# Kernel tuning notes

Measured on AMD Instinct MI355X. Metric: run time of the kernel, lower is better.

The kernel has to match this reference:

```python
import jax, jax.numpy as jnp
import numpy as np

B, S, C = 2, 2048, 512
L, H, CH = 4, 8, 64  # layers, heads, per-head channel (H*CH == C)
OD = 4 * CH          # GEGLU output_dim = channel*4 = 256
EPS = 1e-5


def layer_norm(x, g, b):
    mu = jnp.mean(x, axis=-1, keepdims=True)
    var = jnp.mean(jnp.square(x - mu), axis=-1, keepdims=True)
    return (x - mu) * jax.lax.rsqrt(var + EPS) * g + b


def gelu_tanh(g):
    # matches: 0.5 * g * (1 + tanh(g * 0.7978845608 * (1 + 0.044715 * g**2)))
    t = jnp.tanh(g * 0.7978845608 * (1.0 + 0.044715 * jnp.square(g)))
    return 0.5 * g * (1.0 + t)


def setup_inputs() -> dict:
    key = jax.random.key(0)
    ks = jax.random.split(key, 8)
    s = 0.02
    return {
        "x": jax.random.normal(ks[0], (B, S, C), jnp.float32),
        "ln_gamma": jnp.ones((L + 1, C), jnp.float32),
        "ln_beta": jnp.zeros((L + 1, C), jnp.float32),
        "Wq": jax.random.normal(ks[1], (L, C, H * CH), jnp.float32) * s,
        "Wk": jax.random.normal(ks[2], (L, C, H * CH), jnp.float32) * s,
        "Wv": jax.random.normal(ks[3], (L, C, H * CH), jnp.float32) * s,
        "Wo": jax.random.normal(ks[4], (L, H * CH, C), jnp.float32) * s,
        "bo": jnp.zeros((L, C), jnp.float32),
        "Wg": jax.random.normal(ks[5], (C, 2 * OD), jnp.float32) * s,
        "bg": jnp.zeros((2 * OD,), jnp.float32),
        "Wf": jax.random.normal(ks[6], (OD, C), jnp.float32) * s,
        "bf": jnp.zeros((C,), jnp.float32),
    }


def reference(x, ln_gamma, ln_beta, Wq, Wk, Wv, Wo, bo, Wg, bg, Wf, bf):
    scale = 1.0 / jnp.sqrt(jnp.asarray(CH, x.dtype))
    for i in range(L):
        h = layer_norm(x, ln_gamma[i], ln_beta[i])
        q = (h @ Wq[i]).reshape(B, S, H, CH)
        k = (h @ Wk[i]).reshape(B, S, H, CH)
        v = (h @ Wv[i]).reshape(B, S, H, CH)
        scores = jnp.einsum("bqhc,bkhc->bhqk", q, k) * scale
        w = jax.nn.softmax(scores, axis=-1)
        o = jnp.einsum("bhqk,bkhc->bqhc", w, v).reshape(B, S, H * CH)
        x = o @ Wo[i] + bo[i] + x
    h = layer_norm(x, ln_gamma[L], ln_beta[L])
    g = h @ Wg + bg
    a, gate = g[..., :OD], g[..., OD:]
    ff = a * gelu_tanh(gate)
    return ff @ Wf + bf + x
```

## Files before the change

### kernel.cpp

```cpp
#include <hip/hip_runtime.h>
#include <hip/hip_bf16.h>


typedef __bf16 bf16_t;
typedef __attribute__((ext_vector_type(8))) __bf16 bf16x8;
typedef __attribute__((ext_vector_type(4))) __bf16 bf16x4;
typedef __attribute__((ext_vector_type(4))) float f32x4;

#define MROWS 4096
#define KVSPLIT 2
#define NT 16

static __device__ __forceinline__ void gload_lds16(const void* g, void* l) {
  __builtin_amdgcn_global_load_lds((const __attribute__((address_space(1))) void*)g,
                                   (__attribute__((address_space(3))) void*)l, 16, 0, 0);
}
static __device__ __forceinline__ float fexp2(float x) {
  float r;
  asm("v_exp_f32 %0, %1" : "=v"(r) : "v"(x));
  return r;
}

__global__ __launch_bounds__(256) void ln_kernel(const float* __restrict__ xin,
    const float* __restrict__ gamma, const float* __restrict__ beta,
    bf16_t* __restrict__ hout)
{
  int w = threadIdx.x >> 6, l = threadIdx.x & 63;
  int row = blockIdx.x * 4 + w;
  const float* xr = xin + (size_t)row * 512 + l * 8;
  f32x4 a = *(const f32x4*)xr;
  f32x4 b2 = *(const f32x4*)(xr + 4);
  float s = a[0]+a[1]+a[2]+a[3]+b2[0]+b2[1]+b2[2]+b2[3];
  #pragma unroll
  for (int m = 1; m < 64; m <<= 1) s += __shfl_xor(s, m, 64);
  float mu = s * (1.0f/512.0f);
  float vs = 0.f;
  #pragma unroll
  for (int i = 0; i < 4; i++) { float d = a[i]-mu; vs += d*d; d = b2[i]-mu; vs += d*d; }
  #pragma unroll
  for (int m = 1; m < 64; m <<= 1) vs += __shfl_xor(vs, m, 64);
  float rstd = rsqrtf(vs * (1.0f/512.0f) + 1e-5f);
  const float* gp = gamma + l*8;
  const float* bp = beta + l*8;
  f32x4 g0 = *(const f32x4*)gp, g1 = *(const f32x4*)(gp+4);
  f32x4 p0 = *(const f32x4*)bp, p1 = *(const f32x4*)(bp+4);
  bf16x8 h;
  #pragma unroll
  for (int i = 0; i < 4; i++) {
    h[i]   = (bf16_t)((a[i]-mu)*rstd*g0[i] + p0[i]);
    h[4+i] = (bf16_t)((b2[i]-mu)*rstd*g1[i] + p1[i]);
  }
  *(bf16x8*)(hout + (size_t)row*512 + l*8) = h;
}

__global__ __launch_bounds__(256) void prep_kernel(
    const float* __restrict__ Wq, const float* __restrict__ Wk, const float* __restrict__ Wv,
    const float* __restrict__ Wo, const float* __restrict__ Wg, const float* __restrict__ Wf,
    bf16_t* __restrict__ WqkvT, bf16_t* __restrict__ WoT,
    bf16_t* __restrict__ WgT, bf16_t* __restrict__ WfT)
{
  __shared__ float tile[32][33];
  int z = blockIdx.z;
  const float* src; bf16_t* dst; int K = 512, N = 512;
  if (z < 12) {
    int lay = z & 3, which = z >> 2;
    src = (which == 0 ? Wq : which == 1 ? Wk : Wv) + (size_t)lay*512*512;
    dst = WqkvT + (size_t)lay*1536*512 + (size_t)which*512*512;
  } else if (z < 16) {
    src = Wo + (size_t)(z-12)*512*512;
    dst = WoT + (size_t)(z-12)*512*512;
  } else if (z == 16) { src = Wg; dst = WgT; }
  else { src = Wf; dst = WfT; K = 256; }
  int k0 = blockIdx.y*32, n0 = blockIdx.x*32;
  if (k0 >= K) return;
  int tx = threadIdx.x & 31, ty = threadIdx.x >> 5;
  #pragma unroll
  for (int j = 0; j < 4; j++)
    tile[ty + j*8][tx] = src[(size_t)(k0 + ty + j*8)*N + n0 + tx];
  __syncthreads();
  #pragma unroll
  for (int j = 0; j < 4; j++)
    dst[(size_t)(n0 + ty + j*8)*K + k0 + tx] = (bf16_t)tile[tx][ty + j*8];
}

template<int EPI, int BM, int NX>
__global__ __launch_bounds__(256) void gemm_bt(
    const bf16_t* __restrict__ A, const bf16_t* __restrict__ Bt,
    int N, int K,
    void* __restrict__ Cout, bf16_t* __restrict__ vTout,
    const float* __restrict__ bias, const float* __restrict__ resid, float qscale)
{
  __shared__ bf16_t As[BM*64];
  __shared__ bf16_t Bs[128*64];
  constexpr int MF = BM/32;
  int cpx = gridDim.x >> 3;
  int logical = (blockIdx.x & 7) * cpx + (blockIdx.x >> 3);
  int bx = logical % NX, by = logical / NX;
  int t = threadIdx.x, w = t >> 6, l = t & 63;
  int tm = by * BM, tn = bx * 128;
  int wm = (w >> 1) * (BM/2), wn = (w & 1) * 64;
  f32x4 acc[MF][4] = {};
  int srow = l >> 3;
  int schunk = ((l & 7) ^ srow) * 8;
  for (int k0 = 0; k0 < K; k0 += 64) {
    __syncthreads();
    #pragma unroll
    for (int i = 0; i < BM/32; i++) {
      int rb = i*32 + w*8;
      gload_lds16(A + (size_t)(tm + rb + srow)*K + k0 + schunk, &As[rb*64]);
    }
    #pragma unroll
    for (int i = 0; i < 4; i++) {
      int rb = i*32 + w*8;
      gload_lds16(Bt + (size_t)(tn + rb + srow)*K + k0 + schunk, &Bs[rb*64]);
    }
    __syncthreads();
    #pragma unroll
    for (int kk = 0; kk < 2; kk++) {
      bf16x8 af[MF], bfr[4];
      #pragma unroll
      for (int mf = 0; mf < MF; mf++) {
        int row = wm + mf*16 + (l & 15);
        int off = (kk*32 + (l >> 4)*8) ^ ((row & 7) << 3);
        af[mf] = *(const bf16x8*)&As[row*64 + off];
      }
      #pragma unroll
      for (int nf = 0; nf < 4; nf++) {
        int row = wn + nf*16 + (l & 15);
        int off = (kk*32 + (l >> 4)*8) ^ ((row & 7) << 3);
        bfr[nf] = *(const bf16x8*)&Bs[row*64 + off];
      }
      #pragma unroll
      for (int mf = 0; mf < MF; mf++)
        #pragma unroll
        for (int nf = 0; nf < 4; nf++)
          acc[mf][nf] = __builtin_amdgcn_mfma_f32_16x16x32_bf16(af[mf], bfr[nf], acc[mf][nf], 0, 0, 0);
    }
  }
  int colb = tn + wn + (l & 15);
  int rowb = tm + wm + ((l >> 4) << 2);
  if (EPI == 0 && tn >= 1024) {
    #pragma unroll
    for (int mf = 0; mf < MF; mf++)
      #pragma unroll
      for (int nf = 0; nf < 4; nf++) {
        int col = colb + nf*16;
        int hh = (col - 1024) >> 6, ch = (col - 1024) & 63;
        int row = rowb + mf*16;
        int bb = row >> 11, sdx = row & 2047;
        bf16x4 pk;
        #pragma unroll
        for (int r = 0; r < 4; r++) pk[r] = (bf16_t)acc[mf][nf][r];
        *(bf16x4*)&vTout[(((size_t)bb*8 + hh)*64 + ch)*2048 + sdx] = pk;
      }
    return;
  }
  #pragma unroll
  for (int mf = 0; mf < MF; mf++)
    #pragma unroll
    for (int nf = 0; nf < 4; nf++)
      #pragma unroll
      for (int r = 0; r < 4; r++) {
        int row = rowb + mf*16 + r;
        int col = colb + nf*16;
        float v = acc[mf][nf][r];
        if (EPI == 0) {
          if (col < 512) v *= qscale;
          ((bf16_t*)Cout)[(size_t)row*1024 + col] = (bf16_t)v;
        } else if (EPI == 1) {
          ((float*)Cout)[(size_t)row*N + col] = v + bias[col] + resid[(size_t)row*N + col];
        } else {
          ((float*)Cout)[(size_t)row*N + col] = v + bias[col];
        }
      }
}

__global__ __launch_bounds__(256) void attn_kernel(const bf16_t* __restrict__ qkv,
                                                   const bf16_t* __restrict__ vT,
                                                   bf16_t* __restrict__ Ows,
                                                   float* __restrict__ lws)
{
  __shared__ bf16_t Ks[64*64];
  __shared__ bf16_t Vs[64*64];
  __shared__ bf16_t Ps[4*16*72];
  int t = threadIdx.x, w = t >> 6, l = t & 63;
  int logical = (blockIdx.x & 7) * 128 + (blockIdx.x >> 3);
  int q0 = (logical & 31) * 64;
  int group = logical >> 5;
  int h = group & 7;
  int bz = group >> 3;
  int b = bz >> 1, sp = bz & 1;
  size_t rbase = (size_t)b * 2048;
  int kvb = sp * (2048/KVSPLIT);
  int lq = l & 15, hi = l >> 4;
  int srow = l >> 3;
  int schunk = ((l & 7) ^ srow) * 8;
  int rb0 = w*16, rb1 = w*16 + 8;
  const bf16_t* kb  = qkv + rbase*1024 + 512 + h*64;
  const bf16_t* vtb = vT + ((size_t)(b*8 + h)*64)*2048 + kvb;
  const bf16_t* qp = qkv + (rbase + q0 + w*16 + lq)*1024 + h*64 + hi*8;
  bf16x8 aq0 = *(const bf16x8*)qp;
  bf16x8 aq1 = *(const bf16x8*)(qp + 32);
  gload_lds16(kb + (size_t)(kvb + rb0 + srow)*1024 + schunk, &Ks[rb0*64]);
  gload_lds16(kb + (size_t)(kvb + rb1 + srow)*1024 + schunk, &Ks[rb1*64]);
  gload_lds16(vtb + (size_t)(rb0 + srow)*2048 + schunk, &Vs[rb0*64]);
  gload_lds16(vtb + (size_t)(rb1 + srow)*2048 + schunk, &Vs[rb1*64]);
  asm volatile("s_waitcnt vmcnt(0)" ::: "memory");
  __builtin_amdgcn_s_barrier();

  int pw = w * 16 * 72;
  f32x4 accO[4] = {};
  f32x4 lacc = {};
  bf16x8 ones;
  #pragma unroll
  for (int e = 0; e < 8; e++) ones[e] = (bf16_t)1.0f;
  int swz = (lq & 7) << 3;

  for (int tt = 0; tt < NT; ++tt) {
    f32x4 s4[4] = {};
    bf16x8 vv[8];
    #pragma unroll
    for (int kk = 0; kk < 2; kk++) {
      int off = (kk*32 + hi*8) ^ swz;
      bf16x8 aq = kk ? aq1 : aq0;
      #pragma unroll
      for (int nf = 0; nf < 4; nf++) {
        bf16x8 bk = *(const bf16x8*)&Ks[(nf*16 + lq)*64 + off];
        s4[nf] = __builtin_amdgcn_mfma_f32_16x16x32_bf16(aq, bk, s4[nf], 0, 0, 0);
        vv[kk*4+nf] = *(const bf16x8*)&Vs[(nf*16 + lq)*64 + off];
      }
    }
    asm volatile("s_waitcnt lgkmcnt(0)" ::: "memory");
    __builtin_amdgcn_s_barrier();
    __builtin_amdgcn_sched_barrier(0);
    if (tt < NT-1) {
      int kv1 = kvb + (tt + 1) * 64;
      gload_lds16(kb + (size_t)(kv1 + rb0 + srow)*1024 + schunk, &Ks[rb0*64]);
      gload_lds16(kb + (size_t)(kv1 + rb1 + srow)*1024 + schunk, &Ks[rb1*64]);
      gload_lds16(vtb + (size_t)(rb0 + srow)*2048 + (tt+1)*64 + schunk, &Vs[rb0*64]);
      gload_lds16(vtb + (size_t)(rb1 + srow)*2048 + (tt+1)*64 + schunk, &Vs[rb1*64]);
    }
    #pragma unroll
    for (int nf = 0; nf < 4; nf++)
      #pragma unroll
      for (int r = 0; r < 4; r++)
        Ps[pw + (hi*4 + r)*72 + nf*16 + lq] = (bf16_t)fexp2(s4[nf][r]);
    #pragma unroll
    for (int kk = 0; kk < 2; kk++) {
      bf16x8 pa = *(const bf16x8*)&Ps[pw + lq*72 + kk*32 + hi*8];
      lacc = __builtin_amdgcn_mfma_f32_16x16x32_bf16(pa, ones, lacc, 0, 0, 0);
      #pragma unroll
      for (int nf = 0; nf < 4; nf++)
        accO[nf] = __builtin_amdgcn_mfma_f32_16x16x32_bf16(pa, vv[kk*4+nf], accO[nf], 0, 0, 0);
    }
    if (tt < NT-1) {
      asm volatile("s_waitcnt vmcnt(0)" ::: "memory");
      __builtin_amdgcn_s_barrier();
    }
  }
  bf16_t* op = Ows + (size_t)sp*MROWS*512 + (rbase + q0 + w*16 + hi*4)*512 + h*64 + lq;
  #pragma unroll
  for (int nf = 0; nf < 4; nf++)
    #pragma unroll
    for (int r = 0; r < 4; r++)
      op[(size_t)r*512 + nf*16] = (bf16_t)accO[nf][r];
  if (lq == 0) {
    size_t rowb = rbase + q0 + w*16 + hi*4;
    #pragma unroll
    for (int r = 0; r < 4; r++)
      lws[(size_t)sp*MROWS*8 + (rowb + r)*8 + h] = lacc[r];
  }
}

__global__ __launch_bounds__(256) void combine_kernel(const bf16_t* __restrict__ Ows,
                                                      const float* __restrict__ lws,
                                                      bf16_t* __restrict__ obuf)
{
  int idx = blockIdx.x * 256 + threadIdx.x;
  int row = idx >> 7, c4 = (idx & 127) * 4;
  bf16x4 o0 = *(const bf16x4*)&Ows[(size_t)row*512 + c4];
  bf16x4 o1 = *(const bf16x4*)&Ows[(size_t)(MROWS + row)*512 + c4];
  int h = c4 >> 6;
  float li = 1.0f / (lws[row*8 + h] + lws[MROWS*8 + row*8 + h]);
  bf16x4 o;
  #pragma unroll
  for (int i = 0; i < 4; i++) o[i] = (bf16_t)(((float)o0[i] + (float)o1[i]) * li);
  *(bf16x4*)&obuf[(size_t)row*512 + c4] = o;
}

__global__ __launch_bounds__(256) void gelu_kernel(const float* __restrict__ g,
                                                   bf16_t* __restrict__ ff)
{
  int idx = blockIdx.x * 256 + threadIdx.x;
  int row = idx >> 6;
  int c = (idx & 63) * 4;
  const float* gr = g + (size_t)row*512;
  f32x4 a = *(const f32x4*)(gr + c);
  f32x4 u = *(const f32x4*)(gr + 256 + c);
  bf16x4 o4;
  #pragma unroll
  for (int i = 0; i < 4; i++) {
    float x = u[i];
    float tt = tanhf(0.7978845608f * x * (1.0f + 0.044715f * x * x));
    o4[i] = (bf16_t)(a[i] * 0.5f * x * (1.0f + tt));
  }
  *(bf16x4*)(ff + (size_t)row*256 + c) = o4;
}

extern "C" void kernel_launch(void* const* d_in, const int* in_sizes, int n_in,
                              void* d_out, int out_size, void* d_ws, size_t ws_size,
                              hipStream_t stream)
{
  const float* x     = (const float*)d_in[0];
  const float* gamma = (const float*)d_in[1];
  const float* beta  = (const float*)d_in[2];
  const float* Wq    = (const float*)d_in[3];
  const float* Wk    = (const float*)d_in[4];
  const float* Wv    = (const float*)d_in[5];
  const float* Wo    = (const float*)d_in[6];
  const float* bo    = (const float*)d_in[7];
  const float* Wg    = (const float*)d_in[8];
  const float* bg    = (const float*)d_in[9];
  const float* Wf    = (const float*)d_in[10];
  const float* bf    = (const float*)d_in[11];

  char* ws = (char*)d_ws;
  float*  xcur  = (float*)ws;
  bf16_t* hbuf  = (bf16_t*)(ws + (8u<<20));
  bf16_t* qkv   = (bf16_t*)(ws + (12u<<20));
  bf16_t* vT    = (bf16_t*)(ws + (20u<<20));
  bf16_t* obuf  = (bf16_t*)(ws + (24u<<20));
  bf16_t* WqkvT = (bf16_t*)(ws + (28u<<20));
  bf16_t* WoT   = (bf16_t*)(ws + (34u<<20));
  bf16_t* WgT   = (bf16_t*)(ws + (36u<<20));
  bf16_t* WfT   = (bf16_t*)(ws + (36u<<20) + (512u<<10));
  float*  lws   = (float*)(ws + (37u<<20));
  bf16_t* Ows   = (bf16_t*)(ws + (40u<<20));
  float*  gbuf  = (float*)qkv;
  bf16_t* ffb   = obuf;

  const float QSCALE = 0.125f * 1.44269504f;

  prep_kernel<<<dim3(16,16,18), 256, 0, stream>>>(Wq,Wk,Wv,Wo,Wg,Wf,WqkvT,WoT,WgT,WfT);
  hipMemcpyAsync(xcur, x, (size_t)MROWS*512*4, hipMemcpyDeviceToDevice, stream);

  for (int lay = 0; lay < 4; lay++) {
    ln_kernel<<<1024, 256, 0, stream>>>(xcur, gamma + lay*512, beta + lay*512, hbuf);
    gemm_bt<0,64,12><<<768, 256, 0, stream>>>(hbuf, WqkvT + (size_t)lay*1536*512,
                                              1536, 512, qkv, vT, nullptr, nullptr, QSCALE);
    attn_kernel<<<1024, 256, 0, stream>>>(qkv, vT, Ows, lws);
    combine_kernel<<<2048, 256, 0, stream>>>(Ows, lws, obuf);
    gemm_bt<1,64,4><<<256, 256, 0, stream>>>(obuf, WoT + (size_t)lay*512*512,
                                             512, 512, xcur, nullptr, bo + lay*512, xcur, 1.0f);
  }
  ln_kernel<<<1024, 256, 0, stream>>>(xcur, gamma + 4*512, beta + 4*512, hbuf);
  gemm_bt<2,64,4><<<256, 256, 0, stream>>>(hbuf, WgT, 512, 512, gbuf, nullptr, bg, nullptr, 1.0f);
  gelu_kernel<<<1024, 256, 0, stream>>>(gbuf, ffb);
  gemm_bt<1,64,4><<<256, 256, 0, stream>>>(ffb, WfT, 512, 256, d_out, nullptr, bf, xcur, 1.0f);
}
```

Baseline: 389.4 us.

## Store K and V in pre-tiled per-head blocks; double-buffer K, read V directly

The QKV GEMM epilogue now writes Q to its own buffer and writes K and V into contiguous per-(batch, head, 64-row tile) blocks. Attention can then stream K into a double-buffered LDS tile and load V fragments straight from global memory into registers, with no V staging in LDS. The change removes the mid-iteration barrier and the strided global loads, and it raises wave priority around the MFMA sections. The trade-offs are scattered 2-byte stores for K in the GEMM epilogue and V reads that come from global or cache on every iteration.

```diff
diff --git a/kernel.cpp b/kernel.cpp
--- a/kernel.cpp
+++ b/kernel.cpp
@@ -87,7 +87,7 @@
 __global__ __launch_bounds__(256) void gemm_bt(
     const bf16_t* __restrict__ A, const bf16_t* __restrict__ Bt,
     int N, int K,
-    void* __restrict__ Cout, bf16_t* __restrict__ vTout,
+    void* __restrict__ Cout, bf16_t* __restrict__ kTout, bf16_t* __restrict__ vTout,
     const float* __restrict__ bias, const float* __restrict__ resid, float qscale)
 {
   __shared__ bf16_t As[BM*64];
@@ -147,11 +147,27 @@
         int col = colb + nf*16;
         int hh = (col - 1024) >> 6, ch = (col - 1024) & 63;
         int row = rowb + mf*16;
-        int bb = row >> 11, sdx = row & 2047;
+        int bb = row >> 11, sin = row & 2047;
         bf16x4 pk;
         #pragma unroll
         for (int r = 0; r < 4; r++) pk[r] = (bf16_t)acc[mf][nf][r];
-        *(bf16x4*)&vTout[(((size_t)bb*8 + hh)*64 + ch)*2048 + sdx] = pk;
+        *(bf16x4*)&vTout[(((size_t)(bb*8 + hh)*32 + (sin >> 6))*64 + ch)*64 + (sin & 63)] = pk;
+      }
+    return;
+  }
+  if (EPI == 0 && tn >= 512) {
+    #pragma unroll
+    for (int mf = 0; mf < MF; mf++)
+      #pragma unroll
+      for (int nf = 0; nf < 4; nf++) {
+        int col = colb + nf*16;
+        int hh = (col - 512) >> 6, ch = (col - 512) & 63;
+        int row = rowb + mf*16;
+        int bb = row >> 11, sin = row & 2047;
+        size_t base = (((size_t)(bb*8 + hh)*32 + (sin >> 6))*64 + (sin & 63))*64 + ch;
+        #pragma unroll
+        for (int r = 0; r < 4; r++)
+          kTout[base + (size_t)r*64] = (bf16_t)acc[mf][nf][r];
       }
     return;
   }
@@ -165,8 +181,7 @@
         int col = colb + nf*16;
         float v = acc[mf][nf][r];
         if (EPI == 0) {
-          if (col < 512) v *= qscale;
-          ((bf16_t*)Cout)[(size_t)row*1024 + col] = (bf16_t)v;
+          ((bf16_t*)Cout)[(size_t)row*512 + col] = (bf16_t)(v * qscale);
         } else if (EPI == 1) {
           ((float*)Cout)[(size_t)row*N + col] = v + bias[col] + resid[(size_t)row*N + col];
         } else {
@@ -175,13 +190,13 @@
       }
 }
 
-__global__ __launch_bounds__(256) void attn_kernel(const bf16_t* __restrict__ qkv,
+__global__ __launch_bounds__(256) void attn_kernel(const bf16_t* __restrict__ qbuf,
+                                                   const bf16_t* __restrict__ kT,
                                                    const bf16_t* __restrict__ vT,
                                                    bf16_t* __restrict__ Ows,
                                                    float* __restrict__ lws)
 {
-  __shared__ bf16_t Ks[64*64];
-  __shared__ bf16_t Vs[64*64];
+  __shared__ bf16_t Ks[2][64*64];
   __shared__ bf16_t Ps[4*16*72];
   int t = threadIdx.x, w = t >> 6, l = t & 63;
   int logical = (blockIdx.x & 7) * 128 + (blockIdx.x >> 3);
@@ -191,20 +206,18 @@
   int bz = group >> 3;
   int b = bz >> 1, sp = bz & 1;
   size_t rbase = (size_t)b * 2048;
-  int kvb = sp * (2048/KVSPLIT);
   int lq = l & 15, hi = l >> 4;
   int srow = l >> 3;
   int schunk = ((l & 7) ^ srow) * 8;
   int rb0 = w*16, rb1 = w*16 + 8;
-  const bf16_t* kb  = qkv + rbase*1024 + 512 + h*64;
-  const bf16_t* vtb = vT + ((size_t)(b*8 + h)*64)*2048 + kvb;
-  const bf16_t* qp = qkv + (rbase + q0 + w*16 + lq)*1024 + h*64 + hi*8;
+  size_t tbase = ((size_t)(b*8 + h)*32 + sp*16) * 4096;
+  const bf16_t* kb = kT + tbase;
+  const bf16_t* vb = vT + tbase + (size_t)lq*64 + hi*8;
+  const bf16_t* qp = qbuf + (rbase + q0 + w*16 + lq)*512 + h*64 + hi*8;
   bf16x8 aq0 = *(const bf16x8*)qp;
   bf16x8 aq1 = *(const bf16x8*)(qp + 32);
-  gload_lds16(kb + (size_t)(kvb + rb0 + srow)*1024 + schunk, &Ks[rb0*64]);
-  gload_lds16(kb + (size_t)(kvb + rb1 + srow)*1024 + schunk, &Ks[rb1*64]);
-  gload_lds16(vtb + (size_t)(rb0 + srow)*2048 + schunk, &Vs[rb0*64]);
-  gload_lds16(vtb + (size_t)(rb1 + srow)*2048 + schunk, &Vs[rb1*64]);
+  gload_lds16(kb + (size_t)(rb0 + srow)*64 + schunk, &Ks[0][rb0*64]);
+  gload_lds16(kb + (size_t)(rb1 + srow)*64 + schunk, &Ks[0][rb1*64]);
   asm volatile("s_waitcnt vmcnt(0)" ::: "memory");
   __builtin_amdgcn_s_barrier();
 
@@ -217,34 +230,39 @@
   int swz = (lq & 7) << 3;
 
   for (int tt = 0; tt < NT; ++tt) {
+    int cur = tt & 1;
+    bf16x8 vv[8];
+    const bf16_t* vt0 = vb + (size_t)tt*4096;
+    #pragma unroll
+    for (int nf = 0; nf < 4; nf++) {
+      vv[nf]   = *(const bf16x8*)(vt0 + nf*1024);
+      vv[4+nf] = *(const bf16x8*)(vt0 + nf*1024 + 32);
+    }
+    if (tt < NT-1) {
+      const bf16_t* kn = kb + (size_t)(tt+1)*4096;
+      gload_lds16(kn + (size_t)(rb0 + srow)*64 + schunk, &Ks[cur^1][rb0*64]);
+      gload_lds16(kn + (size_t)(rb1 + srow)*64 + schunk, &Ks[cur^1][rb1*64]);
+    }
+    __builtin_amdgcn_sched_barrier(0);
     f32x4 s4[4] = {};
-    bf16x8 vv[8];
+    __builtin_amdgcn_s_setprio(1);
     #pragma unroll
     for (int kk = 0; kk < 2; kk++) {
       int off = (kk*32 + hi*8) ^ swz;
       bf16x8 aq = kk ? aq1 : aq0;
       #pragma unroll
       for (int nf = 0; nf < 4; nf++) {
-        bf16x8 bk = *(const bf16x8*)&Ks[(nf*16 + lq)*64 + off];
+        bf16x8 bk = *(const bf16x8*)&Ks[cur][(nf*16 + lq)*64 + off];
         s4[nf] = __builtin_amdgcn_mfma_f32_16x16x32_bf16(aq, bk, s4[nf], 0, 0, 0);
-        vv[kk*4+nf] = *(const bf16x8*)&Vs[(nf*16 + lq)*64 + off];
-      }
-    }
-    asm volatile("s_waitcnt lgkmcnt(0)" ::: "memory");
-    __builtin_amdgcn_s_barrier();
-    __builtin_amdgcn_sched_barrier(0);
-    if (tt < NT-1) {
-      int kv1 = kvb + (tt + 1) * 64;
-      gload_lds16(kb + (size_t)(kv1 + rb0 + srow)*1024 + schunk, &Ks[rb0*64]);
-      gload_lds16(kb + (size_t)(kv1 + rb1 + srow)*1024 + schunk, &Ks[rb1*64]);
-      gload_lds16(vtb + (size_t)(rb0 + srow)*2048 + (tt+1)*64 + schunk, &Vs[rb0*64]);
-      gload_lds16(vtb + (size_t)(rb1 + srow)*2048 + (tt+1)*64 + schunk, &Vs[rb1*64]);
-    }
+      }
+    }
+    __builtin_amdgcn_s_setprio(0);
     #pragma unroll
     for (int nf = 0; nf < 4; nf++)
       #pragma unroll
       for (int r = 0; r < 4; r++)
         Ps[pw + (hi*4 + r)*72 + nf*16 + lq] = (bf16_t)fexp2(s4[nf][r]);
+    __builtin_amdgcn_s_setprio(1);
     #pragma unroll
     for (int kk = 0; kk < 2; kk++) {
       bf16x8 pa = *(const bf16x8*)&Ps[pw + lq*72 + kk*32 + hi*8];
@@ -253,8 +271,9 @@
       for (int nf = 0; nf < 4; nf++)
         accO[nf] = __builtin_amdgcn_mfma_f32_16x16x32_bf16(pa, vv[kk*4+nf], accO[nf], 0, 0, 0);
     }
+    __builtin_amdgcn_s_setprio(0);
     if (tt < NT-1) {
-      asm volatile("s_waitcnt vmcnt(0)" ::: "memory");
+      asm volatile("s_waitcnt vmcnt(0) lgkmcnt(0)" ::: "memory");
       __builtin_amdgcn_s_barrier();
     }
   }
@@ -327,8 +346,9 @@
   char* ws = (char*)d_ws;
   float*  xcur  = (float*)ws;
   bf16_t* hbuf  = (bf16_t*)(ws + (8u<<20));
-  bf16_t* qkv   = (bf16_t*)(ws + (12u<<20));
-  bf16_t* vT    = (bf16_t*)(ws + (20u<<20));
+  bf16_t* qbuf  = (bf16_t*)(ws + (12u<<20));
+  bf16_t* kTb   = (bf16_t*)(ws + (16u<<20));
+  bf16_t* vTb   = (bf16_t*)(ws + (20u<<20));
   bf16_t* obuf  = (bf16_t*)(ws + (24u<<20));
   bf16_t* WqkvT = (bf16_t*)(ws + (28u<<20));
   bf16_t* WoT   = (bf16_t*)(ws + (34u<<20));
@@ -336,7 +356,7 @@
   bf16_t* WfT   = (bf16_t*)(ws + (36u<<20) + (512u<<10));
   float*  lws   = (float*)(ws + (37u<<20));
   bf16_t* Ows   = (bf16_t*)(ws + (40u<<20));
-  float*  gbuf  = (float*)qkv;
+  float*  gbuf  = (float*)(ws + (40u<<20));
   bf16_t* ffb   = obuf;
 
   const float QSCALE = 0.125f * 1.44269504f;
@@ -347,14 +367,14 @@
   for (int lay = 0; lay < 4; lay++) {
     ln_kernel<<<1024, 256, 0, stream>>>(xcur, gamma + lay*512, beta + lay*512, hbuf);
     gemm_bt<0,64,12><<<768, 256, 0, stream>>>(hbuf, WqkvT + (size_t)lay*1536*512,
-                                              1536, 512, qkv, vT, nullptr, nullptr, QSCALE);
-    attn_kernel<<<1024, 256, 0, stream>>>(qkv, vT, Ows, lws);
+                                              1536, 512, qbuf, kTb, vTb, nullptr, nullptr, QSCALE);
+    attn_kernel<<<1024, 256, 0, stream>>>(qbuf, kTb, vTb, Ows, lws);
     combine_kernel<<<2048, 256, 0, stream>>>(Ows, lws, obuf);
     gemm_bt<1,64,4><<<256, 256, 0, stream>>>(obuf, WoT + (size_t)lay*512*512,
-                                             512, 512, xcur, nullptr, bo + lay*512, xcur, 1.0f);
+                                             512, 512, xcur, nullptr, nullptr, bo + lay*512, xcur, 1.0f);
   }
   ln_kernel<<<1024, 256, 0, stream>>>(xcur, gamma + 4*512, beta + 4*512, hbuf);
-  gemm_bt<2,64,4><<<256, 256, 0, stream>>>(hbuf, WgT, 512, 512, gbuf, nullptr, bg, nullptr, 1.0f);
+  gemm_bt<2,64,4><<<256, 256, 0, stream>>>(hbuf, WgT, 512, 512, gbuf, nullptr, nullptr, bg, nullptr, 1.0f);
   gelu_kernel<<<1024, 256, 0, stream>>>(gbuf, ffb);
-  gemm_bt<1,64,4><<<256, 256, 0, stream>>>(ffb, WfT, 512, 256, d_out, nullptr, bf, xcur, 1.0f);
-}
+  gemm_bt<1,64,4><<<256, 256, 0, stream>>>(ffb, WfT, 512, 256, d_out, nullptr, nullptr, bf, xcur, 1.0f);
+}
```

Measured after the change: 518.7 us. +33.2%, slower.
